# Optimization experiments

Hardware: AMD Instinct MI355X
Metric: run time of the kernel (lower is better)

The kernel has to match this reference:

```python
import jax, jax.numpy as jnp
import numpy as np

B, N, E, ED, H, HID, OUT = 128, 100, 3200, 8, 4, 16, 32


def _ln(x, g, b):
    m = x.mean(-1, keepdims=True)
    v = ((x - m) ** 2).mean(-1, keepdims=True)
    return (x - m) / jnp.sqrt(v + 1e-5) * g + b


def _seg_softmax(logits, seg, n):
    # logits: [Etot, H], seg: [Etot] target node ids
    m = jax.ops.segment_max(logits, seg, num_segments=n)
    ex = jnp.exp(logits - m[seg])
    s = jax.ops.segment_sum(ex, seg, num_segments=n)
    return ex / (s[seg] + 1e-16)


def _tconv(x, src, dst, ea, Wq, bq, Wk, bk, Wv, bv, We, Ws, bs, heads, ch, n):
    # PyG TransformerConv, concat=False, root_weight=True, beta=False
    q = (x @ Wq.T + bq).reshape(-1, heads, ch)
    k = (x @ Wk.T + bk).reshape(-1, heads, ch)
    v = (x @ Wv.T + bv).reshape(-1, heads, ch)
    e = (ea @ We.T).reshape(-1, heads, ch)
    alpha = (q[dst] * (k[src] + e)).sum(-1) / jnp.sqrt(jnp.float32(ch))  # [Etot,H]
    alpha = _seg_softmax(alpha, dst, n)
    msg = (v[src] + e) * alpha[..., None]
    out = jax.ops.segment_sum(msg, dst, num_segments=n)  # [n,H,ch]
    out = out.mean(axis=1)  # concat=False -> head mean
    return out + x @ Ws.T + bs


def setup_inputs() -> dict:
    key = jax.random.key(0)
    ks = jax.random.split(key, 32)
    d = {}
    d['nodes_feats'] = jax.random.randint(ks[0], (B, N, 1), 0, 5).astype(jnp.float32)
    d['edge_index'] = jax.random.randint(ks[1], (B, 2, E), 0, N).astype(jnp.int32)
    d['edge_attr'] = jax.random.normal(ks[2], (B, E, ED), jnp.float32)
    d['agent_id'] = jax.random.randint(ks[3], (B, 1), 0, N).astype(jnp.int32)
    s = 0.1
    d['entity_embed'] = jax.random.normal(ks[4], (5, 4), jnp.float32)
    d['W1'] = jax.random.normal(ks[5], (HID, 4 + ED), jnp.float32) * s
    d['b1'] = jnp.zeros((HID,), jnp.float32)
    d['W2'] = jax.random.normal(ks[6], (HID, HID), jnp.float32) * s
    d['b2'] = jnp.zeros((HID,), jnp.float32)
    d['W3'] = jax.random.normal(ks[7], (HID, HID), jnp.float32) * s
    d['b3'] = jnp.zeros((HID,), jnp.float32)
    d['ln_g'] = jnp.ones((HID,), jnp.float32)
    d['ln_b'] = jnp.zeros((HID,), jnp.float32)
    i = 8
    for pre, ch, outd in (('g1', HID, HID), ('g2', OUT, OUT)):
        d[pre + '_Wq'] = jax.random.normal(ks[i + 0], (H * ch, HID), jnp.float32) * s
        d[pre + '_bq'] = jnp.zeros((H * ch,), jnp.float32)
        d[pre + '_Wk'] = jax.random.normal(ks[i + 1], (H * ch, HID), jnp.float32) * s
        d[pre + '_bk'] = jnp.zeros((H * ch,), jnp.float32)
        d[pre + '_Wv'] = jax.random.normal(ks[i + 2], (H * ch, HID), jnp.float32) * s
        d[pre + '_bv'] = jnp.zeros((H * ch,), jnp.float32)
        d[pre + '_We'] = jax.random.normal(ks[i + 3], (H * ch, ED), jnp.float32) * s
        d[pre + '_Ws'] = jax.random.normal(ks[i + 4], (outd, HID), jnp.float32) * s
        d[pre + '_bs'] = jnp.zeros((outd,), jnp.float32)
        i += 5
    return d


def reference(nodes_feats, edge_index, edge_attr, agent_id, entity_embed,
              W1, b1, W2, b2, W3, b3, ln_g, ln_b,
              g1_Wq, g1_bq, g1_Wk, g1_bk, g1_Wv, g1_bv, g1_We, g1_Ws, g1_bs,
              g2_Wq, g2_bq, g2_Wk, g2_bk, g2_Wv, g2_bv, g2_We, g2_Ws, g2_bs):
    n_tot = B * N
    # batched graph -> flat graph with per-batch node offsets
    offs = (jnp.arange(B, dtype=edge_index.dtype) * N)[:, None, None]
    ei = (edge_index + offs).transpose(1, 0, 2).reshape(2, -1)  # [2, B*E]
    src, dst = ei[0], ei[1]
    x = nodes_feats.reshape(-1, 1)            # [n_tot, 1]
    ea = edge_attr.reshape(-1, ED)            # [B*E, ED]

    # Embedding message-passing layer (aggr='add')
    etype = x[:, 0].astype(jnp.int32)[src]
    emb = entity_embed[etype]                  # [Etot, 4]
    h = jnp.concatenate([emb, ea], axis=1)
    h = _ln(jax.nn.relu(h @ W1.T + b1), ln_g, ln_b)
    h = _ln(jax.nn.relu(h @ W2.T + b2), ln_g, ln_b)
    h = _ln(jax.nn.relu(h @ W3.T + b3), ln_g, ln_b)
    z = jax.ops.segment_sum(h, dst, num_segments=n_tot)  # [n_tot, 16]

    a = _tconv(z, src, dst, ea, g1_Wq, g1_bq, g1_Wk, g1_bk, g1_Wv, g1_bv,
               g1_We, g1_Ws, g1_bs, H, HID, n_tot)
    a = _tconv(a, src, dst, ea, g2_Wq, g2_bq, g2_Wk, g2_bk, g2_Wv, g2_bv,
               g2_We, g2_Ws, g2_bs, H, OUT, n_tot)
    a = jax.nn.relu(a).reshape(B, N, OUT)
    # graph_aggr == 'agent': gather the agent node per batch
    out = jnp.take_along_axis(a, agent_id[:, :, None].astype(jnp.int32), axis=1)
    return out[:, 0, :]  # [B, OUT]
```

## Files before the change

### kernel.cpp

```cpp
#include <hip/hip_runtime.h>
#include <math.h>
#include <stdint.h>

#define Bb   128
#define Nn   100
#define Ee   3200
#define NTOT (Bb*Nn)
#define ETOT (Bb*Ee)



__global__ __launch_bounds__(256) void k_csr(const int* __restrict__ ei,
                                             const int* __restrict__ agent,
                                             int* __restrict__ off,
                                             int2* __restrict__ cpair,
                                             int* __restrict__ mark)
{
    int b = ((blockIdx.x & 7) << 4) + (blockIdx.x >> 3);
    int t = threadIdx.x;
    __shared__ int cnt[128];
    __shared__ int exc[128];
    __shared__ int cur[128];
    if (t < 128) cnt[t] = 0;
    if (t < Nn) mark[b * Nn + t] = 0;
    __syncthreads();
    const int* eis = ei + (size_t)b * 2 * Ee;
    const int* eid = eis + Ee;
    for (int e = t; e < Ee; e += 256) atomicAdd(&cnt[eid[e]], 1);
    __syncthreads();
    if (t < 128) exc[t] = cnt[t];
    __syncthreads();
    for (int d = 1; d < 128; d <<= 1) {
        int v = 0;
        if (t < 128 && t >= d) v = exc[t - d];
        __syncthreads();
        if (t < 128) exc[t] += v;
        __syncthreads();
    }
    if (t < 128) { int e0 = exc[t] - cnt[t]; exc[t] = e0; cur[t] = e0; }
    __syncthreads();
    if (t < Nn) off[b * Nn + t] = b * Ee + exc[t];
    if (b == Bb - 1 && t == 0) off[NTOT] = ETOT;
    for (int e = t; e < Ee; e += 256) {
        int dst = eid[e];
        int idx = atomicAdd(&cur[dst], 1);
        cpair[b * Ee + idx] = make_int2(eis[e] + b * Nn, b * Ee + e);
    }
    int an = agent[b];
    __syncthreads();
    if (t == 0) mark[b * Nn + an] = 1;
    for (int e = t; e < Ee; e += 256) {
        if (eid[e] == an) mark[b * Nn + eis[e]] = 1;
    }
}


__device__ __forceinline__ void ln_reg(float* h, const float* __restrict__ g,
                                       const float* __restrict__ b) {
    float s = 0.f;
#pragma unroll
    for (int c = 0; c < 16; c++) s += h[c];
    float m = s * 0.0625f;
    float v = 0.f;
#pragma unroll
    for (int c = 0; c < 16; c++) { float d = h[c] - m; v += d * d; }
    float r = rsqrtf(v * 0.0625f + 1e-5f);
#pragma unroll
    for (int c = 0; c < 16; c++) h[c] = (h[c] - m) * r * g[c] + b[c];
}

__global__ __launch_bounds__(256) void k_mlpz(
    const float* __restrict__ nf, const float* __restrict__ ea, const float* __restrict__ ee,
    const float* __restrict__ W1, const float* __restrict__ b1,
    const float* __restrict__ W2, const float* __restrict__ b2,
    const float* __restrict__ W3, const float* __restrict__ b3,
    const float* __restrict__ lg, const float* __restrict__ lb,
    const float* __restrict__ Wq, const float* __restrict__ bq,
    const float* __restrict__ Wk, const float* __restrict__ bk,
    const float* __restrict__ Wv, const float* __restrict__ bv,
    const int* __restrict__ off, const int2* __restrict__ cpair,
    float* __restrict__ z, float* __restrict__ q1, float* __restrict__ k1, float* __restrict__ v1)
{
    __shared__ float hs[4][64][17];
    __shared__ int sdeg[4];
    int lane = threadIdx.x & 63;
    int wid  = threadIdx.x >> 6;
    int n    = (blockIdx.x & 7) * (NTOT / 8) + (blockIdx.x >> 3) * 4 + wid;

    int o0 = off[n];
    int deg = off[n + 1] - o0;
    if (lane == 0) sdeg[wid] = deg;
    __syncthreads();
    int mdeg = max(max(sdeg[0], sdeg[1]), max(sdeg[2], sdeg[3]));
    int chunks = (mdeg + 63) >> 6;

    float zp = 0.f;
    for (int ch = 0; ch < chunks; ch++) {
        int i = ch * 64 + lane;
        float h3[16];
        if (i < deg) {
            int2 p = cpair[o0 + i];
            int et = (int)nf[p.x];
            float in[12];
#pragma unroll
            for (int j = 0; j < 4; j++) in[j] = ee[et * 4 + j];
            const float4* ea4 = (const float4*)(ea + (size_t)p.y * 8);
            float4 ua = ea4[0], ub = ea4[1];
            in[4] = ua.x; in[5] = ua.y; in[6] = ua.z; in[7] = ua.w;
            in[8] = ub.x; in[9] = ub.y; in[10] = ub.z; in[11] = ub.w;

            float h1[16];
#pragma unroll
            for (int c = 0; c < 16; c++) {
                float s = b1[c];
#pragma unroll
                for (int j = 0; j < 12; j++) s = fmaf(W1[c * 12 + j], in[j], s);
                h1[c] = fmaxf(s, 0.f);
            }
            ln_reg(h1, lg, lb);
            float h2[16];
#pragma unroll
            for (int c = 0; c < 16; c++) {
                float s = b2[c];
#pragma unroll
                for (int j = 0; j < 16; j++) s = fmaf(W2[c * 16 + j], h1[j], s);
                h2[c] = fmaxf(s, 0.f);
            }
            ln_reg(h2, lg, lb);
#pragma unroll
            for (int c = 0; c < 16; c++) {
                float s = b3[c];
#pragma unroll
                for (int j = 0; j < 16; j++) s = fmaf(W3[c * 16 + j], h2[j], s);
                h3[c] = fmaxf(s, 0.f);
            }
            ln_reg(h3, lg, lb);
        } else {
#pragma unroll
            for (int c = 0; c < 16; c++) h3[c] = 0.f;
        }
#pragma unroll
        for (int c = 0; c < 16; c++) hs[wid][lane][c] = h3[c];
        __syncthreads();
        int g = lane >> 4, c = lane & 15;
        float s = 0.f;
#pragma unroll
        for (int k = 0; k < 16; k++) s += hs[wid][g * 16 + k][c];
        s += __shfl_xor(s, 16);
        s += __shfl_xor(s, 32);
        zp += s;
        __syncthreads();
    }

    if (lane < 16) z[n * 16 + lane] = zp;

    float aq = bq[lane], ak = bk[lane], av = bv[lane];
#pragma unroll
    for (int j = 0; j < 16; j++) {
        float zj = __shfl(zp, j, 16);
        aq = fmaf(Wq[lane * 16 + j], zj, aq);
        ak = fmaf(Wk[lane * 16 + j], zj, ak);
        av = fmaf(Wv[lane * 16 + j], zj, av);
    }
    q1[n * 64 + lane] = aq;
    k1[n * 64 + lane] = ak;
    v1[n * 64 + lane] = av;
}


__global__ __launch_bounds__(256) void k_attn1(
    const float* __restrict__ ea,
    const float* __restrict__ q1, const float* __restrict__ k1, const float* __restrict__ v1,
    const float* __restrict__ We, const float* __restrict__ Ws, const float* __restrict__ bs,
    const float* __restrict__ z, const int* __restrict__ mark,
    const int* __restrict__ off, const int2* __restrict__ cpair,
    float* __restrict__ a1)
{
    int lane = threadIdx.x & 63;
    int wid  = threadIdx.x >> 6;
    int n    = (blockIdx.x & 7) * (NTOT / 8) + (blockIdx.x >> 3) * 4 + wid;

    if (!mark[n]) return;

    float wer[8];
#pragma unroll
    for (int j = 0; j < 8; j++) wer[j] = We[lane * 8 + j];
    float ql = q1[n * 64 + lane];

    int o0 = off[n];
    int deg = off[n + 1] - o0;

    float m = -1e30f, l = 0.f, acc = 0.f;
    int i = 0;
    for (; i + 2 <= deg; i += 2) {
        int2 pA = cpair[o0 + i];
        int2 pB = cpair[o0 + i + 1];
        const float4* eaA = (const float4*)(ea + (size_t)pA.y * 8);
        const float4* eaB = (const float4*)(ea + (size_t)pB.y * 8);
        float4 a0v = eaA[0], a1v = eaA[1], b0v = eaB[0], b1v = eaB[1];
        float eA = wer[0] * a0v.x + wer[1] * a0v.y + wer[2] * a0v.z + wer[3] * a0v.w
                 + wer[4] * a1v.x + wer[5] * a1v.y + wer[6] * a1v.z + wer[7] * a1v.w;
        float eB = wer[0] * b0v.x + wer[1] * b0v.y + wer[2] * b0v.z + wer[3] * b0v.w
                 + wer[4] * b1v.x + wer[5] * b1v.y + wer[6] * b1v.z + wer[7] * b1v.w;
        float kA = k1[(size_t)pA.x * 64 + lane];
        float kB = k1[(size_t)pB.x * 64 + lane];
        float vA = v1[(size_t)pA.x * 64 + lane];
        float vB = v1[(size_t)pB.x * 64 + lane];
        float tA = ql * (kA + eA);
        float tB = ql * (kB + eB);
        tA += __shfl_xor(tA, 1, 16);  tB += __shfl_xor(tB, 1, 16);
        tA += __shfl_xor(tA, 2, 16);  tB += __shfl_xor(tB, 2, 16);
        tA += __shfl_xor(tA, 4, 16);  tB += __shfl_xor(tB, 4, 16);
        tA += __shfl_xor(tA, 8, 16);  tB += __shfl_xor(tB, 8, 16);
        float lA = tA * 0.25f;
        float lB = tB * 0.25f;
        float nm = fmaxf(m, fmaxf(lA, lB));
        float sc = __expf(m - nm);
        float wA = __expf(lA - nm);
        float wB = __expf(lB - nm);
        acc = acc * sc + wA * (vA + eA) + wB * (vB + eB);
        l   = l * sc + wA + wB;
        m   = nm;
    }
    for (; i < deg; i++) {
        int2 p = cpair[o0 + i];
        const float4* ea4 = (const float4*)(ea + (size_t)p.y * 8);
        float4 u0 = ea4[0], u1 = ea4[1];
        float el = wer[0] * u0.x + wer[1] * u0.y + wer[2] * u0.z + wer[3] * u0.w
                 + wer[4] * u1.x + wer[5] * u1.y + wer[6] * u1.z + wer[7] * u1.w;
        float kl = k1[(size_t)p.x * 64 + lane];
        float t = ql * (kl + el);
        t += __shfl_xor(t, 1, 16);
        t += __shfl_xor(t, 2, 16);
        t += __shfl_xor(t, 4, 16);
        t += __shfl_xor(t, 8, 16);
        float logit = t * 0.25f;
        float nm = fmaxf(m, logit);
        float sc = __expf(m - nm);
        float w  = __expf(logit - nm);
        float vl = v1[(size_t)p.x * 64 + lane];
        acc = acc * sc + w * (vl + el);
        l   = l * sc + w;
        m   = nm;
    }
    float y = (deg > 0) ? (acc / l) : 0.f;
    y += __shfl_xor(y, 16);
    y += __shfl_xor(y, 32);
    y *= 0.25f;

    if (lane < 16) {
        float r = bs[lane];
#pragma unroll
        for (int j = 0; j < 16; j++) r = fmaf(Ws[lane * 16 + j], z[n * 16 + j], r);
        a1[n * 16 + lane] = y + r;
    }
}


__global__ __launch_bounds__(256) void k_g2(
    const float* __restrict__ ea, const float* __restrict__ a1, const int* __restrict__ agent,
    const float* __restrict__ Wq, const float* __restrict__ bq,
    const float* __restrict__ Wk, const float* __restrict__ bk,
    const float* __restrict__ Wv, const float* __restrict__ bv,
    const float* __restrict__ We, const float* __restrict__ Ws, const float* __restrict__ bs,
    const int* __restrict__ off, const int2* __restrict__ cpair,
    float* __restrict__ out)
{
    __shared__ float sm[4][64], sl[4][64], sa0[4][64], sa1[4][64];
    int b = ((blockIdx.x & 7) << 4) + (blockIdx.x >> 3);
    int lane = threadIdx.x & 63;
    int w = threadIdx.x >> 6;
    int n = b * Nn + agent[b];
    int v0 = lane * 2, v1i = lane * 2 + 1;

    float aa[16];
#pragma unroll
    for (int j = 0; j < 16; j++) aa[j] = a1[n * 16 + j];

    float wk0[16], wk1[16], wv0[16], wv1[16], we0[8], we1[8];
#pragma unroll
    for (int j = 0; j < 16; j++) {
        wk0[j] = Wk[v0 * 16 + j];  wk1[j] = Wk[v1i * 16 + j];
        wv0[j] = Wv[v0 * 16 + j];  wv1[j] = Wv[v1i * 16 + j];
    }
#pragma unroll
    for (int j = 0; j < 8; j++) { we0[j] = We[v0 * 8 + j]; we1[j] = We[v1i * 8 + j]; }

    float q0 = bq[v0], q1v = bq[v1i];
#pragma unroll
    for (int j = 0; j < 16; j++) {
        q0  = fmaf(Wq[v0 * 16 + j],  aa[j], q0);
        q1v = fmaf(Wq[v1i * 16 + j], aa[j], q1v);
    }

    int o0 = off[n];
    int deg = off[n + 1] - o0;

    float m = -1e30f, l = 0.f, a0 = 0.f, a1c = 0.f;
    for (int i = w; i < deg; i += 4) {
        int2 p = cpair[o0 + i];
        int src = p.x, ge = p.y;
        float as[16];
#pragma unroll
        for (int j = 0; j < 16; j++) as[j] = a1[src * 16 + j];
        const float4* ea4 = (const float4*)(ea + (size_t)ge * 8);
        float4 u0 = ea4[0], u1 = ea4[1];
        float eav[8] = {u0.x, u0.y, u0.z, u0.w, u1.x, u1.y, u1.z, u1.w};

        float k0 = bk[v0], k1v = bk[v1i], vv0 = bv[v0], vv1 = bv[v1i];
#pragma unroll
        for (int j = 0; j < 16; j++) {
            k0  = fmaf(wk0[j], as[j], k0);
            k1v = fmaf(wk1[j], as[j], k1v);
            vv0 = fmaf(wv0[j], as[j], vv0);
            vv1 = fmaf(wv1[j], as[j], vv1);
        }
        float e0 = 0.f, e1 = 0.f;
#pragma unroll
        for (int j = 0; j < 8; j++) { e0 = fmaf(we0[j], eav[j], e0); e1 = fmaf(we1[j], eav[j], e1); }

        float t = q0 * (k0 + e0) + q1v * (k1v + e1);
        t += __shfl_xor(t, 1, 16);
        t += __shfl_xor(t, 2, 16);
        t += __shfl_xor(t, 4, 16);
        t += __shfl_xor(t, 8, 16);
        float logit = t * 0.17677669529663687f;
        float nm = fmaxf(m, logit);
        float sc = __expf(m - nm);
        float wgt = __expf(logit - nm);
        a0  = a0 * sc + wgt * (vv0 + e0);
        a1c = a1c * sc + wgt * (vv1 + e1);
        l   = l * sc + wgt;
        m   = nm;
    }
    sm[w][lane] = m; sl[w][lane] = l; sa0[w][lane] = a0; sa1[w][lane] = a1c;
    __syncthreads();
    if (w == 0) {
        float M = fmaxf(fmaxf(sm[0][lane], sm[1][lane]), fmaxf(sm[2][lane], sm[3][lane]));
        float L = 0.f, A0 = 0.f, A1 = 0.f;
#pragma unroll
        for (int ww = 0; ww < 4; ww++) {
            float sc = __expf(sm[ww][lane] - M);
            L  += sc * sl[ww][lane];
            A0 += sc * sa0[ww][lane];
            A1 += sc * sa1[ww][lane];
        }
        float y0 = (deg > 0) ? (A0 / L) : 0.f;
        float y1 = (deg > 0) ? (A1 / L) : 0.f;
        y0 += __shfl_xor(y0, 16); y0 += __shfl_xor(y0, 32);
        y1 += __shfl_xor(y1, 16); y1 += __shfl_xor(y1, 32);
        y0 *= 0.25f; y1 *= 0.25f;

        if (lane < 16) {
            int c0 = lane * 2, c1 = lane * 2 + 1;
            float r0 = bs[c0], r1 = bs[c1];
#pragma unroll
            for (int j = 0; j < 16; j++) {
                r0 = fmaf(Ws[c0 * 16 + j], aa[j], r0);
                r1 = fmaf(Ws[c1 * 16 + j], aa[j], r1);
            }
            out[b * 32 + c0] = fmaxf(y0 + r0, 0.f);
            out[b * 32 + c1] = fmaxf(y1 + r1, 0.f);
        }
    }
}


extern "C" void kernel_launch(void* const* d_in, const int* in_sizes, int n_in,
                              void* d_out, int out_size, void* d_ws, size_t ws_size,
                              hipStream_t stream) {
    (void)in_sizes; (void)n_in; (void)out_size; (void)ws_size;
    const float* nf    = (const float*)d_in[0];
    const int*   ei    = (const int*)d_in[1];
    const float* ea    = (const float*)d_in[2];
    const int*   agent = (const int*)d_in[3];
    const float* ee    = (const float*)d_in[4];
    const float* W1    = (const float*)d_in[5];
    const float* b1    = (const float*)d_in[6];
    const float* W2    = (const float*)d_in[7];
    const float* b2    = (const float*)d_in[8];
    const float* W3    = (const float*)d_in[9];
    const float* b3    = (const float*)d_in[10];
    const float* lg    = (const float*)d_in[11];
    const float* lb    = (const float*)d_in[12];
    const float* g1Wq  = (const float*)d_in[13];
    const float* g1bq  = (const float*)d_in[14];
    const float* g1Wk  = (const float*)d_in[15];
    const float* g1bk  = (const float*)d_in[16];
    const float* g1Wv  = (const float*)d_in[17];
    const float* g1bv  = (const float*)d_in[18];
    const float* g1We  = (const float*)d_in[19];
    const float* g1Ws  = (const float*)d_in[20];
    const float* g1bs  = (const float*)d_in[21];
    const float* g2Wq  = (const float*)d_in[22];
    const float* g2bq  = (const float*)d_in[23];
    const float* g2Wk  = (const float*)d_in[24];
    const float* g2bk  = (const float*)d_in[25];
    const float* g2Wv  = (const float*)d_in[26];
    const float* g2bv  = (const float*)d_in[27];
    const float* g2We  = (const float*)d_in[28];
    const float* g2Ws  = (const float*)d_in[29];
    const float* g2bs  = (const float*)d_in[30];
    float* out = (float*)d_out;

    char* w = (char*)d_ws;
    int* mark  = (int*)w;  w += (size_t)NTOT * 4;
    int* off   = (int*)w;  w += (size_t)(NTOT + 4) * 4;
    w = (char*)(((uintptr_t)w + 15) & ~(uintptr_t)15);
    int2* cpair = (int2*)w; w += (size_t)ETOT * 8;
    float* z   = (float*)w; w += (size_t)NTOT * 16 * 4;
    float* q1  = (float*)w; w += (size_t)NTOT * 64 * 4;
    float* k1  = (float*)w; w += (size_t)NTOT * 64 * 4;
    float* v1  = (float*)w; w += (size_t)NTOT * 64 * 4;
    float* a1  = (float*)w; w += (size_t)NTOT * 16 * 4;

    k_csr<<<dim3(Bb), dim3(256), 0, stream>>>(ei, agent, off, cpair, mark);
    k_mlpz<<<dim3(NTOT / 4), dim3(256), 0, stream>>>(
        nf, ea, ee, W1, b1, W2, b2, W3, b3, lg, lb,
        g1Wq, g1bq, g1Wk, g1bk, g1Wv, g1bv,
        off, cpair, z, q1, k1, v1);
    k_attn1<<<dim3(NTOT / 4), dim3(256), 0, stream>>>(
        ea, q1, k1, v1, g1We, g1Ws, g1bs, z, mark, off, cpair, a1);
    k_g2<<<dim3(Bb), dim3(256), 0, stream>>>(
        ea, a1, agent, g2Wq, g2bq, g2Wk, g2bk, g2Wv, g2bv, g2We, g2Ws, g2bs,
        off, cpair, out);
}
```

Before: 204.6 us.

## Fuse CSR build, edge MLP, both attention layers into one per-graph kernel

Replaces four launches with a single kernel using one 512-thread block per graph. CSR offsets, the marked-node list, z and the layer-1 outputs live in shared memory. The edge MLP now runs over edges in their original order and accumulates into z with shared-memory atomics instead of a CSR-gathered per-node reduction. This removes launch overhead and global round-trips for z, q, mark, offsets and a1, and computes q only for marked nodes. The cost is that only 128 blocks run, which limits occupancy across the GPU's compute units, and all nodes' k/v still go through global memory.

```diff
diff --git a/kernel.cpp b/kernel.cpp
--- a/kernel.cpp
+++ b/kernel.cpp
@@ -7,26 +7,67 @@
 #define Ee   3200
 #define NTOT (Bb*Nn)
 #define ETOT (Bb*Ee)
-
-
-
-__global__ __launch_bounds__(256) void k_csr(const int* __restrict__ ei,
-                                             const int* __restrict__ agent,
-                                             int* __restrict__ off,
-                                             int2* __restrict__ cpair,
-                                             int* __restrict__ mark)
+#define NT   512
+
+
+__device__ __forceinline__ void ln_reg(float* h, const float* __restrict__ g,
+                                       const float* __restrict__ b) {
+    float s = 0.f;
+#pragma unroll
+    for (int c = 0; c < 16; c++) s += h[c];
+    float m = s * 0.0625f;
+    float v = 0.f;
+#pragma unroll
+    for (int c = 0; c < 16; c++) { float d = h[c] - m; v += d * d; }
+    float r = rsqrtf(v * 0.0625f + 1e-5f);
+#pragma unroll
+    for (int c = 0; c < 16; c++) h[c] = (h[c] - m) * r * g[c] + b[c];
+}
+
+__global__ __launch_bounds__(NT) void k_all(
+    const float* __restrict__ nf, const int* __restrict__ ei,
+    const float* __restrict__ ea, const int* __restrict__ agent,
+    const float* __restrict__ ee,
+    const float* __restrict__ W1, const float* __restrict__ b1,
+    const float* __restrict__ W2, const float* __restrict__ b2,
+    const float* __restrict__ W3, const float* __restrict__ b3,
+    const float* __restrict__ lg, const float* __restrict__ lb,
+    const float* __restrict__ Wq1, const float* __restrict__ bq1,
+    const float* __restrict__ Wk1, const float* __restrict__ bk1,
+    const float* __restrict__ Wv1, const float* __restrict__ bv1,
+    const float* __restrict__ We1, const float* __restrict__ Ws1,
+    const float* __restrict__ bs1,
+    const float* __restrict__ Wq2, const float* __restrict__ bq2,
+    const float* __restrict__ Wk2, const float* __restrict__ bk2,
+    const float* __restrict__ Wv2, const float* __restrict__ bv2,
+    const float* __restrict__ We2, const float* __restrict__ Ws2,
+    const float* __restrict__ bs2,
+    int2* __restrict__ cpair, float* __restrict__ k1, float* __restrict__ v1,
+    float* __restrict__ out)
 {
-    int b = ((blockIdx.x & 7) << 4) + (blockIdx.x >> 3);
+    __shared__ float zs[Nn * 17];
+    __shared__ float a1s[Nn * 16];
+    __shared__ int cnt[128], exc[128], cur[128];
+    __shared__ int offl[Nn + 1];
+    __shared__ int markf[Nn];
+    __shared__ int list[Nn];
+    __shared__ int nmark;
+    __shared__ float sm[8][64], sl[8][64], sa0[8][64], sa1[8][64];
+
+    int b = blockIdx.x;
     int t = threadIdx.x;
-    __shared__ int cnt[128];
-    __shared__ int exc[128];
-    __shared__ int cur[128];
-    if (t < 128) cnt[t] = 0;
-    if (t < Nn) mark[b * Nn + t] = 0;
-    __syncthreads();
+    int lane = t & 63;
+    int w = t >> 6;
     const int* eis = ei + (size_t)b * 2 * Ee;
     const int* eid = eis + Ee;
-    for (int e = t; e < Ee; e += 256) atomicAdd(&cnt[eid[e]], 1);
+
+    for (int i = t; i < 128; i += NT) cnt[i] = 0;
+    for (int i = t; i < Nn; i += NT) markf[i] = 0;
+    for (int i = t; i < Nn * 17; i += NT) zs[i] = 0.f;
+    if (t == 0) nmark = 0;
+    __syncthreads();
+
+    for (int e = t; e < Ee; e += NT) atomicAdd(&cnt[eid[e]], 1);
     __syncthreads();
     if (t < 128) exc[t] = cnt[t];
     __syncthreads();
@@ -39,328 +80,254 @@
     }
     if (t < 128) { int e0 = exc[t] - cnt[t]; exc[t] = e0; cur[t] = e0; }
     __syncthreads();
-    if (t < Nn) off[b * Nn + t] = b * Ee + exc[t];
-    if (b == Bb - 1 && t == 0) off[NTOT] = ETOT;
-    for (int e = t; e < Ee; e += 256) {
-        int dst = eid[e];
+    if (t <= Nn) offl[t] = exc[t];
+    int an = agent[b];
+    for (int e = t; e < Ee; e += NT) {
+        int dst = eid[e], src = eis[e];
         int idx = atomicAdd(&cur[dst], 1);
-        cpair[b * Ee + idx] = make_int2(eis[e] + b * Nn, b * Ee + e);
-    }
-    int an = agent[b];
-    __syncthreads();
-    if (t == 0) mark[b * Nn + an] = 1;
-    for (int e = t; e < Ee; e += 256) {
-        if (eid[e] == an) mark[b * Nn + eis[e]] = 1;
-    }
-}
-
-
-__device__ __forceinline__ void ln_reg(float* h, const float* __restrict__ g,
-                                       const float* __restrict__ b) {
-    float s = 0.f;
-#pragma unroll
-    for (int c = 0; c < 16; c++) s += h[c];
-    float m = s * 0.0625f;
-    float v = 0.f;
-#pragma unroll
-    for (int c = 0; c < 16; c++) { float d = h[c] - m; v += d * d; }
-    float r = rsqrtf(v * 0.0625f + 1e-5f);
-#pragma unroll
-    for (int c = 0; c < 16; c++) h[c] = (h[c] - m) * r * g[c] + b[c];
-}
-
-__global__ __launch_bounds__(256) void k_mlpz(
-    const float* __restrict__ nf, const float* __restrict__ ea, const float* __restrict__ ee,
-    const float* __restrict__ W1, const float* __restrict__ b1,
-    const float* __restrict__ W2, const float* __restrict__ b2,
-    const float* __restrict__ W3, const float* __restrict__ b3,
-    const float* __restrict__ lg, const float* __restrict__ lb,
-    const float* __restrict__ Wq, const float* __restrict__ bq,
-    const float* __restrict__ Wk, const float* __restrict__ bk,
-    const float* __restrict__ Wv, const float* __restrict__ bv,
-    const int* __restrict__ off, const int2* __restrict__ cpair,
-    float* __restrict__ z, float* __restrict__ q1, float* __restrict__ k1, float* __restrict__ v1)
-{
-    __shared__ float hs[4][64][17];
-    __shared__ int sdeg[4];
-    int lane = threadIdx.x & 63;
-    int wid  = threadIdx.x >> 6;
-    int n    = (blockIdx.x & 7) * (NTOT / 8) + (blockIdx.x >> 3) * 4 + wid;
-
-    int o0 = off[n];
-    int deg = off[n + 1] - o0;
-    if (lane == 0) sdeg[wid] = deg;
-    __syncthreads();
-    int mdeg = max(max(sdeg[0], sdeg[1]), max(sdeg[2], sdeg[3]));
-    int chunks = (mdeg + 63) >> 6;
-
-    float zp = 0.f;
-    for (int ch = 0; ch < chunks; ch++) {
-        int i = ch * 64 + lane;
+        cpair[(size_t)b * Ee + idx] = make_int2(src, e);
+        if (dst == an) markf[src] = 1;
+    }
+    if (t == 0) markf[an] = 1;
+    __syncthreads();
+    if (t < Nn && markf[t]) { int i = atomicAdd(&nmark, 1); list[i] = t; }
+
+    for (int e = t; e < Ee; e += NT) {
+        int src = eis[e], dst = eid[e];
+        int et = (int)nf[b * Nn + src];
+        float in[12];
+#pragma unroll
+        for (int j = 0; j < 4; j++) in[j] = ee[et * 4 + j];
+        const float4* ea4 = (const float4*)(ea + ((size_t)b * Ee + e) * 8);
+        float4 ua = ea4[0], ub = ea4[1];
+        in[4] = ua.x; in[5] = ua.y; in[6] = ua.z; in[7] = ua.w;
+        in[8] = ub.x; in[9] = ub.y; in[10] = ub.z; in[11] = ub.w;
+
+        float h1[16];
+#pragma unroll
+        for (int c = 0; c < 16; c++) {
+            float s = b1[c];
+#pragma unroll
+            for (int j = 0; j < 12; j++) s = fmaf(W1[c * 12 + j], in[j], s);
+            h1[c] = fmaxf(s, 0.f);
+        }
+        ln_reg(h1, lg, lb);
+        float h2[16];
+#pragma unroll
+        for (int c = 0; c < 16; c++) {
+            float s = b2[c];
+#pragma unroll
+            for (int j = 0; j < 16; j++) s = fmaf(W2[c * 16 + j], h1[j], s);
+            h2[c] = fmaxf(s, 0.f);
+        }
+        ln_reg(h2, lg, lb);
         float h3[16];
-        if (i < deg) {
-            int2 p = cpair[o0 + i];
-            int et = (int)nf[p.x];
-            float in[12];
-#pragma unroll
-            for (int j = 0; j < 4; j++) in[j] = ee[et * 4 + j];
-            const float4* ea4 = (const float4*)(ea + (size_t)p.y * 8);
-            float4 ua = ea4[0], ub = ea4[1];
-            in[4] = ua.x; in[5] = ua.y; in[6] = ua.z; in[7] = ua.w;
-            in[8] = ub.x; in[9] = ub.y; in[10] = ub.z; in[11] = ub.w;
-
-            float h1[16];
-#pragma unroll
-            for (int c = 0; c < 16; c++) {
-                float s = b1[c];
-#pragma unroll
-                for (int j = 0; j < 12; j++) s = fmaf(W1[c * 12 + j], in[j], s);
-                h1[c] = fmaxf(s, 0.f);
-            }
-            ln_reg(h1, lg, lb);
-            float h2[16];
-#pragma unroll
-            for (int c = 0; c < 16; c++) {
-                float s = b2[c];
-#pragma unroll
-                for (int j = 0; j < 16; j++) s = fmaf(W2[c * 16 + j], h1[j], s);
-                h2[c] = fmaxf(s, 0.f);
-            }
-            ln_reg(h2, lg, lb);
-#pragma unroll
-            for (int c = 0; c < 16; c++) {
-                float s = b3[c];
-#pragma unroll
-                for (int j = 0; j < 16; j++) s = fmaf(W3[c * 16 + j], h2[j], s);
-                h3[c] = fmaxf(s, 0.f);
-            }
-            ln_reg(h3, lg, lb);
-        } else {
-#pragma unroll
-            for (int c = 0; c < 16; c++) h3[c] = 0.f;
-        }
-#pragma unroll
-        for (int c = 0; c < 16; c++) hs[wid][lane][c] = h3[c];
+#pragma unroll
+        for (int c = 0; c < 16; c++) {
+            float s = b3[c];
+#pragma unroll
+            for (int j = 0; j < 16; j++) s = fmaf(W3[c * 16 + j], h2[j], s);
+            h3[c] = fmaxf(s, 0.f);
+        }
+        ln_reg(h3, lg, lb);
+#pragma unroll
+        for (int c = 0; c < 16; c++) atomicAdd(&zs[dst * 17 + c], h3[c]);
+    }
+    __syncthreads();
+
+    {
+        float wkr[16], wvr[16];
+#pragma unroll
+        for (int j = 0; j < 16; j++) { wkr[j] = Wk1[lane * 16 + j]; wvr[j] = Wv1[lane * 16 + j]; }
+        float bkl = bk1[lane], bvl = bv1[lane];
+        for (int base = 0; base < Nn; base += 8) {
+            int n = base + w;
+            if (n < Nn) {
+                float ak = bkl, av = bvl;
+#pragma unroll
+                for (int j = 0; j < 16; j++) {
+                    float zj = zs[n * 17 + j];
+                    ak = fmaf(wkr[j], zj, ak);
+                    av = fmaf(wvr[j], zj, av);
+                }
+                size_t o = ((size_t)b * Nn + n) * 64 + lane;
+                k1[o] = ak;
+                v1[o] = av;
+            }
+        }
+    }
+    __syncthreads();
+
+    {
+        int nmk = nmark;
+        float wer[8];
+#pragma unroll
+        for (int j = 0; j < 8; j++) wer[j] = We1[lane * 8 + j];
+        float wqr[16];
+#pragma unroll
+        for (int j = 0; j < 16; j++) wqr[j] = Wq1[lane * 16 + j];
+        float bql = bq1[lane];
+
+        for (int li = w; li < nmk; li += 8) {
+            int n = list[li];
+            float ql = bql;
+#pragma unroll
+            for (int j = 0; j < 16; j++) ql = fmaf(wqr[j], zs[n * 17 + j], ql);
+            int o0 = offl[n], deg = offl[n + 1] - o0;
+            const int2* cp = cpair + (size_t)b * Ee + o0;
+            const float* kb = k1 + (size_t)b * Nn * 64;
+            const float* vb = v1 + (size_t)b * Nn * 64;
+
+            float m = -1e30f, l = 0.f, acc = 0.f;
+            int i = 0;
+            for (; i + 2 <= deg; i += 2) {
+                int2 pA = cp[i], pB = cp[i + 1];
+                const float4* eaA = (const float4*)(ea + ((size_t)b * Ee + pA.y) * 8);
+                const float4* eaB = (const float4*)(ea + ((size_t)b * Ee + pB.y) * 8);
+                float4 a0v = eaA[0], a1v = eaA[1], b0v = eaB[0], b1v = eaB[1];
+                float eA = wer[0]*a0v.x + wer[1]*a0v.y + wer[2]*a0v.z + wer[3]*a0v.w
+                         + wer[4]*a1v.x + wer[5]*a1v.y + wer[6]*a1v.z + wer[7]*a1v.w;
+                float eB = wer[0]*b0v.x + wer[1]*b0v.y + wer[2]*b0v.z + wer[3]*b0v.w
+                         + wer[4]*b1v.x + wer[5]*b1v.y + wer[6]*b1v.z + wer[7]*b1v.w;
+                float kA = kb[(size_t)pA.x * 64 + lane];
+                float kB = kb[(size_t)pB.x * 64 + lane];
+                float vA = vb[(size_t)pA.x * 64 + lane];
+                float vB = vb[(size_t)pB.x * 64 + lane];
+                float tA = ql * (kA + eA);
+                float tB = ql * (kB + eB);
+                tA += __shfl_xor(tA, 1, 16);  tB += __shfl_xor(tB, 1, 16);
+                tA += __shfl_xor(tA, 2, 16);  tB += __shfl_xor(tB, 2, 16);
+                tA += __shfl_xor(tA, 4, 16);  tB += __shfl_xor(tB, 4, 16);
+                tA += __shfl_xor(tA, 8, 16);  tB += __shfl_xor(tB, 8, 16);
+                float lA = tA * 0.25f;
+                float lB = tB * 0.25f;
+                float nm = fmaxf(m, fmaxf(lA, lB));
+                float sc = __expf(m - nm);
+                float wA = __expf(lA - nm);
+                float wB = __expf(lB - nm);
+                acc = acc * sc + wA * (vA + eA) + wB * (vB + eB);
+                l   = l * sc + wA + wB;
+                m   = nm;
+            }
+            for (; i < deg; i++) {
+                int2 p = cp[i];
+                const float4* ea4 = (const float4*)(ea + ((size_t)b * Ee + p.y) * 8);
+                float4 u0 = ea4[0], u1 = ea4[1];
+                float el = wer[0]*u0.x + wer[1]*u0.y + wer[2]*u0.z + wer[3]*u0.w
+                         + wer[4]*u1.x + wer[5]*u1.y + wer[6]*u1.z + wer[7]*u1.w;
+                float kl = kb[(size_t)p.x * 64 + lane];
+                float tq = ql * (kl + el);
+                tq += __shfl_xor(tq, 1, 16);
+                tq += __shfl_xor(tq, 2, 16);
+                tq += __shfl_xor(tq, 4, 16);
+                tq += __shfl_xor(tq, 8, 16);
+                float logit = tq * 0.25f;
+                float nm = fmaxf(m, logit);
+                float sc = __expf(m - nm);
+                float wt = __expf(logit - nm);
+                float vl = vb[(size_t)p.x * 64 + lane];
+                acc = acc * sc + wt * (vl + el);
+                l   = l * sc + wt;
+                m   = nm;
+            }
+            float y = (deg > 0) ? (acc / l) : 0.f;
+            y += __shfl_xor(y, 16);
+            y += __shfl_xor(y, 32);
+            y *= 0.25f;
+            if (lane < 16) {
+                float r = bs1[lane];
+#pragma unroll
+                for (int j = 0; j < 16; j++) r = fmaf(Ws1[lane * 16 + j], zs[n * 17 + j], r);
+                a1s[n * 16 + lane] = y + r;
+            }
+        }
+    }
+    __syncthreads();
+
+    {
+        int o0 = offl[an], deg = offl[an + 1] - o0;
+        int c0 = lane * 2, c1 = c0 + 1;
+        float wk0[16], wk1r[16], wv0[16], wv1r[16], we0[8], we1[8];
+#pragma unroll
+        for (int j = 0; j < 16; j++) {
+            wk0[j] = Wk2[c0 * 16 + j];  wk1r[j] = Wk2[c1 * 16 + j];
+            wv0[j] = Wv2[c0 * 16 + j];  wv1r[j] = Wv2[c1 * 16 + j];
+        }
+#pragma unroll
+        for (int j = 0; j < 8; j++) { we0[j] = We2[c0 * 8 + j]; we1[j] = We2[c1 * 8 + j]; }
+        float q0 = bq2[c0], q1v = bq2[c1];
+#pragma unroll
+        for (int j = 0; j < 16; j++) {
+            float aj = a1s[an * 16 + j];
+            q0  = fmaf(Wq2[c0 * 16 + j], aj, q0);
+            q1v = fmaf(Wq2[c1 * 16 + j], aj, q1v);
+        }
+        const int2* cp = cpair + (size_t)b * Ee + o0;
+
+        float m = -1e30f, l = 0.f, a0 = 0.f, a1c = 0.f;
+        for (int i = w; i < deg; i += 8) {
+            int2 p = cp[i];
+            int srcl = p.x;
+            const float4* ea4 = (const float4*)(ea + ((size_t)b * Ee + p.y) * 8);
+            float4 u0 = ea4[0], u1 = ea4[1];
+            float k0 = bk2[c0], k1e = bk2[c1], vv0 = bv2[c0], vv1 = bv2[c1];
+#pragma unroll
+            for (int j = 0; j < 16; j++) {
+                float aj = a1s[srcl * 16 + j];
+                k0  = fmaf(wk0[j],  aj, k0);
+                k1e = fmaf(wk1r[j], aj, k1e);
+                vv0 = fmaf(wv0[j],  aj, vv0);
+                vv1 = fmaf(wv1r[j], aj, vv1);
+            }
+            float e0 = we0[0]*u0.x + we0[1]*u0.y + we0[2]*u0.z + we0[3]*u0.w
+                     + we0[4]*u1.x + we0[5]*u1.y + we0[6]*u1.z + we0[7]*u1.w;
+            float e1 = we1[0]*u0.x + we1[1]*u0.y + we1[2]*u0.z + we1[3]*u0.w
+                     + we1[4]*u1.x + we1[5]*u1.y + we1[6]*u1.z + we1[7]*u1.w;
+            float tq = q0 * (k0 + e0) + q1v * (k1e + e1);
+            tq += __shfl_xor(tq, 1, 16);
+            tq += __shfl_xor(tq, 2, 16);
+            tq += __shfl_xor(tq, 4, 16);
+            tq += __shfl_xor(tq, 8, 16);
+            float logit = tq * 0.17677669529663687f;
+            float nm = fmaxf(m, logit);
+            float sc = __expf(m - nm);
+            float wt = __expf(logit - nm);
+            a0  = a0 * sc + wt * (vv0 + e0);
+            a1c = a1c * sc + wt * (vv1 + e1);
+            l   = l * sc + wt;
+            m   = nm;
+        }
+        sm[w][lane] = m; sl[w][lane] = l; sa0[w][lane] = a0; sa1[w][lane] = a1c;
         __syncthreads();
-        int g = lane >> 4, c = lane & 15;
-        float s = 0.f;
-#pragma unroll
-        for (int k = 0; k < 16; k++) s += hs[wid][g * 16 + k][c];
-        s += __shfl_xor(s, 16);
-        s += __shfl_xor(s, 32);
-        zp += s;
-        __syncthreads();
-    }
-
-    if (lane < 16) z[n * 16 + lane] = zp;
-
-    float aq = bq[lane], ak = bk[lane], av = bv[lane];
-#pragma unroll
-    for (int j = 0; j < 16; j++) {
-        float zj = __shfl(zp, j, 16);
-        aq = fmaf(Wq[lane * 16 + j], zj, aq);
-        ak = fmaf(Wk[lane * 16 + j], zj, ak);
-        av = fmaf(Wv[lane * 16 + j], zj, av);
-    }
-    q1[n * 64 + lane] = aq;
-    k1[n * 64 + lane] = ak;
-    v1[n * 64 + lane] = av;
-}
-
-
-__global__ __launch_bounds__(256) void k_attn1(
-    const float* __restrict__ ea,
-    const float* __restrict__ q1, const float* __restrict__ k1, const float* __restrict__ v1,
-    const float* __restrict__ We, const float* __restrict__ Ws, const float* __restrict__ bs,
-    const float* __restrict__ z, const int* __restrict__ mark,
-    const int* __restrict__ off, const int2* __restrict__ cpair,
-    float* __restrict__ a1)
-{
-    int lane = threadIdx.x & 63;
-    int wid  = threadIdx.x >> 6;
-    int n    = (blockIdx.x & 7) * (NTOT / 8) + (blockIdx.x >> 3) * 4 + wid;
-
-    if (!mark[n]) return;
-
-    float wer[8];
-#pragma unroll
-    for (int j = 0; j < 8; j++) wer[j] = We[lane * 8 + j];
-    float ql = q1[n * 64 + lane];
-
-    int o0 = off[n];
-    int deg = off[n + 1] - o0;
-
-    float m = -1e30f, l = 0.f, acc = 0.f;
-    int i = 0;
-    for (; i + 2 <= deg; i += 2) {
-        int2 pA = cpair[o0 + i];
-        int2 pB = cpair[o0 + i + 1];
-        const float4* eaA = (const float4*)(ea + (size_t)pA.y * 8);
-        const float4* eaB = (const float4*)(ea + (size_t)pB.y * 8);
-        float4 a0v = eaA[0], a1v = eaA[1], b0v = eaB[0], b1v = eaB[1];
-        float eA = wer[0] * a0v.x + wer[1] * a0v.y + wer[2] * a0v.z + wer[3] * a0v.w
-                 + wer[4] * a1v.x + wer[5] * a1v.y + wer[6] * a1v.z + wer[7] * a1v.w;
-        float eB = wer[0] * b0v.x + wer[1] * b0v.y + wer[2] * b0v.z + wer[3] * b0v.w
-                 + wer[4] * b1v.x + wer[5] * b1v.y + wer[6] * b1v.z + wer[7] * b1v.w;
-        float kA = k1[(size_t)pA.x * 64 + lane];
-        float kB = k1[(size_t)pB.x * 64 + lane];
-        float vA = v1[(size_t)pA.x * 64 + lane];
-        float vB = v1[(size_t)pB.x * 64 + lane];
-        float tA = ql * (kA + eA);
-        float tB = ql * (kB + eB);
-        tA += __shfl_xor(tA, 1, 16);  tB += __shfl_xor(tB, 1, 16);
-        tA += __shfl_xor(tA, 2, 16);  tB += __shfl_xor(tB, 2, 16);
-        tA += __shfl_xor(tA, 4, 16);  tB += __shfl_xor(tB, 4, 16);
-        tA += __shfl_xor(tA, 8, 16);  tB += __shfl_xor(tB, 8, 16);
-        float lA = tA * 0.25f;
-        float lB = tB * 0.25f;
-        float nm = fmaxf(m, fmaxf(lA, lB));
-        float sc = __expf(m - nm);
-        float wA = __expf(lA - nm);
-        float wB = __expf(lB - nm);
-        acc = acc * sc + wA * (vA + eA) + wB * (vB + eB);
-        l   = l * sc + wA + wB;
-        m   = nm;
-    }
-    for (; i < deg; i++) {
-        int2 p = cpair[o0 + i];
-        const float4* ea4 = (const float4*)(ea + (size_t)p.y * 8);
-        float4 u0 = ea4[0], u1 = ea4[1];
-        float el = wer[0] * u0.x + wer[1] * u0.y + wer[2] * u0.z + wer[3] * u0.w
-                 + wer[4] * u1.x + wer[5] * u1.y + wer[6] * u1.z + wer[7] * u1.w;
-        float kl = k1[(size_t)p.x * 64 + lane];
-        float t = ql * (kl + el);
-        t += __shfl_xor(t, 1, 16);
-        t += __shfl_xor(t, 2, 16);
-        t += __shfl_xor(t, 4, 16);
-        t += __shfl_xor(t, 8, 16);
-        float logit = t * 0.25f;
-        float nm = fmaxf(m, logit);
-        float sc = __expf(m - nm);
-        float w  = __expf(logit - nm);
-        float vl = v1[(size_t)p.x * 64 + lane];
-        acc = acc * sc + w * (vl + el);
-        l   = l * sc + w;
-        m   = nm;
-    }
-    float y = (deg > 0) ? (acc / l) : 0.f;
-    y += __shfl_xor(y, 16);
-    y += __shfl_xor(y, 32);
-    y *= 0.25f;
-
-    if (lane < 16) {
-        float r = bs[lane];
-#pragma unroll
-        for (int j = 0; j < 16; j++) r = fmaf(Ws[lane * 16 + j], z[n * 16 + j], r);
-        a1[n * 16 + lane] = y + r;
-    }
-}
-
-
-__global__ __launch_bounds__(256) void k_g2(
-    const float* __restrict__ ea, const float* __restrict__ a1, const int* __restrict__ agent,
-    const float* __restrict__ Wq, const float* __restrict__ bq,
-    const float* __restrict__ Wk, const float* __restrict__ bk,
-    const float* __restrict__ Wv, const float* __restrict__ bv,
-    const float* __restrict__ We, const float* __restrict__ Ws, const float* __restrict__ bs,
-    const int* __restrict__ off, const int2* __restrict__ cpair,
-    float* __restrict__ out)
-{
-    __shared__ float sm[4][64], sl[4][64], sa0[4][64], sa1[4][64];
-    int b = ((blockIdx.x & 7) << 4) + (blockIdx.x >> 3);
-    int lane = threadIdx.x & 63;
-    int w = threadIdx.x >> 6;
-    int n = b * Nn + agent[b];
-    int v0 = lane * 2, v1i = lane * 2 + 1;
-
-    float aa[16];
-#pragma unroll
-    for (int j = 0; j < 16; j++) aa[j] = a1[n * 16 + j];
-
-    float wk0[16], wk1[16], wv0[16], wv1[16], we0[8], we1[8];
-#pragma unroll
-    for (int j = 0; j < 16; j++) {
-        wk0[j] = Wk[v0 * 16 + j];  wk1[j] = Wk[v1i * 16 + j];
-        wv0[j] = Wv[v0 * 16 + j];  wv1[j] = Wv[v1i * 16 + j];
-    }
-#pragma unroll
-    for (int j = 0; j < 8; j++) { we0[j] = We[v0 * 8 + j]; we1[j] = We[v1i * 8 + j]; }
-
-    float q0 = bq[v0], q1v = bq[v1i];
-#pragma unroll
-    for (int j = 0; j < 16; j++) {
-        q0  = fmaf(Wq[v0 * 16 + j],  aa[j], q0);
-        q1v = fmaf(Wq[v1i * 16 + j], aa[j], q1v);
-    }
-
-    int o0 = off[n];
-    int deg = off[n + 1] - o0;
-
-    float m = -1e30f, l = 0.f, a0 = 0.f, a1c = 0.f;
-    for (int i = w; i < deg; i += 4) {
-        int2 p = cpair[o0 + i];
-        int src = p.x, ge = p.y;
-        float as[16];
-#pragma unroll
-        for (int j = 0; j < 16; j++) as[j] = a1[src * 16 + j];
-        const float4* ea4 = (const float4*)(ea + (size_t)ge * 8);
-        float4 u0 = ea4[0], u1 = ea4[1];
-        float eav[8] = {u0.x, u0.y, u0.z, u0.w, u1.x, u1.y, u1.z, u1.w};
-
-        float k0 = bk[v0], k1v = bk[v1i], vv0 = bv[v0], vv1 = bv[v1i];
-#pragma unroll
-        for (int j = 0; j < 16; j++) {
-            k0  = fmaf(wk0[j], as[j], k0);
-            k1v = fmaf(wk1[j], as[j], k1v);
-            vv0 = fmaf(wv0[j], as[j], vv0);
-            vv1 = fmaf(wv1[j], as[j], vv1);
-        }
-        float e0 = 0.f, e1 = 0.f;
-#pragma unroll
-        for (int j = 0; j < 8; j++) { e0 = fmaf(we0[j], eav[j], e0); e1 = fmaf(we1[j], eav[j], e1); }
-
-        float t = q0 * (k0 + e0) + q1v * (k1v + e1);
-        t += __shfl_xor(t, 1, 16);
-        t += __shfl_xor(t, 2, 16);
-        t += __shfl_xor(t, 4, 16);
-        t += __shfl_xor(t, 8, 16);
-        float logit = t * 0.17677669529663687f;
-        float nm = fmaxf(m, logit);
-        float sc = __expf(m - nm);
-        float wgt = __expf(logit - nm);
-        a0  = a0 * sc + wgt * (vv0 + e0);
-        a1c = a1c * sc + wgt * (vv1 + e1);
-        l   = l * sc + wgt;
-        m   = nm;
-    }
-    sm[w][lane] = m; sl[w][lane] = l; sa0[w][lane] = a0; sa1[w][lane] = a1c;
-    __syncthreads();
-    if (w == 0) {
-        float M = fmaxf(fmaxf(sm[0][lane], sm[1][lane]), fmaxf(sm[2][lane], sm[3][lane]));
-        float L = 0.f, A0 = 0.f, A1 = 0.f;
-#pragma unroll
-        for (int ww = 0; ww < 4; ww++) {
-            float sc = __expf(sm[ww][lane] - M);
-            L  += sc * sl[ww][lane];
-            A0 += sc * sa0[ww][lane];
-            A1 += sc * sa1[ww][lane];
-        }
-        float y0 = (deg > 0) ? (A0 / L) : 0.f;
-        float y1 = (deg > 0) ? (A1 / L) : 0.f;
-        y0 += __shfl_xor(y0, 16); y0 += __shfl_xor(y0, 32);
-        y1 += __shfl_xor(y1, 16); y1 += __shfl_xor(y1, 32);
-        y0 *= 0.25f; y1 *= 0.25f;
-
-        if (lane < 16) {
-            int c0 = lane * 2, c1 = lane * 2 + 1;
-            float r0 = bs[c0], r1 = bs[c1];
-#pragma unroll
-            for (int j = 0; j < 16; j++) {
-                r0 = fmaf(Ws[c0 * 16 + j], aa[j], r0);
-                r1 = fmaf(Ws[c1 * 16 + j], aa[j], r1);
-            }
-            out[b * 32 + c0] = fmaxf(y0 + r0, 0.f);
-            out[b * 32 + c1] = fmaxf(y1 + r1, 0.f);
+        if (w == 0) {
+            float M = sm[0][lane];
+#pragma unroll
+            for (int ww = 1; ww < 8; ww++) M = fmaxf(M, sm[ww][lane]);
+            float L = 0.f, A0 = 0.f, A1 = 0.f;
+#pragma unroll
+            for (int ww = 0; ww < 8; ww++) {
+                float sc = __expf(sm[ww][lane] - M);
+                L  += sc * sl[ww][lane];
+                A0 += sc * sa0[ww][lane];
+                A1 += sc * sa1[ww][lane];
+            }
+            float y0 = (deg > 0) ? (A0 / L) : 0.f;
+            float y1 = (deg > 0) ? (A1 / L) : 0.f;
+            y0 += __shfl_xor(y0, 16); y0 += __shfl_xor(y0, 32);
+            y1 += __shfl_xor(y1, 16); y1 += __shfl_xor(y1, 32);
+            y0 *= 0.25f; y1 *= 0.25f;
+            if (lane < 16) {
+                int d0 = lane * 2, d1 = d0 + 1;
+                float r0 = bs2[d0], r1 = bs2[d1];
+#pragma unroll
+                for (int j = 0; j < 16; j++) {
+                    float aj = a1s[an * 16 + j];
+                    r0 = fmaf(Ws2[d0 * 16 + j], aj, r0);
+                    r1 = fmaf(Ws2[d1 * 16 + j], aj, r1);
+                }
+                out[b * 32 + d0] = fmaxf(y0 + r0, 0.f);
+                out[b * 32 + d1] = fmaxf(y1 + r1, 0.f);
+            }
         }
     }
 }
@@ -404,24 +371,14 @@
     float* out = (float*)d_out;
 
     char* w = (char*)d_ws;
-    int* mark  = (int*)w;  w += (size_t)NTOT * 4;
-    int* off   = (int*)w;  w += (size_t)(NTOT + 4) * 4;
-    w = (char*)(((uintptr_t)w + 15) & ~(uintptr_t)15);
     int2* cpair = (int2*)w; w += (size_t)ETOT * 8;
-    float* z   = (float*)w; w += (size_t)NTOT * 16 * 4;
-    float* q1  = (float*)w; w += (size_t)NTOT * 64 * 4;
     float* k1  = (float*)w; w += (size_t)NTOT * 64 * 4;
     float* v1  = (float*)w; w += (size_t)NTOT * 64 * 4;
-    float* a1  = (float*)w; w += (size_t)NTOT * 16 * 4;
-
-    k_csr<<<dim3(Bb), dim3(256), 0, stream>>>(ei, agent, off, cpair, mark);
-    k_mlpz<<<dim3(NTOT / 4), dim3(256), 0, stream>>>(
-        nf, ea, ee, W1, b1, W2, b2, W3, b3, lg, lb,
-        g1Wq, g1bq, g1Wk, g1bk, g1Wv, g1bv,
-        off, cpair, z, q1, k1, v1);
-    k_attn1<<<dim3(NTOT / 4), dim3(256), 0, stream>>>(
-        ea, q1, k1, v1, g1We, g1Ws, g1bs, z, mark, off, cpair, a1);
-    k_g2<<<dim3(Bb), dim3(256), 0, stream>>>(
-        ea, a1, agent, g2Wq, g2bq, g2Wk, g2bk, g2Wv, g2bv, g2We, g2Ws, g2bs,
-        off, cpair, out);
+
+    k_all<<<dim3(Bb), dim3(NT), 0, stream>>>(
+        nf, ei, ea, agent, ee,
+        W1, b1, W2, b2, W3, b3, lg, lb,
+        g1Wq, g1bq, g1Wk, g1bk, g1Wv, g1bv, g1We, g1Ws, g1bs,
+        g2Wq, g2bq, g2Wk, g2bk, g2Wv, g2bv, g2We, g2Ws, g2bs,
+        cpair, k1, v1, out);
 }
```

New measurement: 419.5 us. 105% more time.
